# Kernel optimization log

Hardware: AMD Instinct MI355X
Metric: run time of the kernel (lower is better)

Reference implementation:

```python
import jax, jax.numpy as jnp
import numpy as np
from jax import lax

C = 128
HEADS = 8
HID = 256  # int(C * 2.0)
B, H, W = 8, 128, 128
EPS_LN = 1e-5
EPS_NORM = 1e-12


def _dwconv(x, w, pad):
    # x: [B,C,H,W], w: [C,1,kh,kw] depthwise
    return lax.conv_general_dilated(
        x, w, window_strides=(1, 1), padding=[(pad, pad), (pad, pad)],
        dimension_numbers=("NCHW", "OIHW", "NCHW"), feature_group_count=x.shape[1])


def _conv1x1(x, w):
    # w: [O, I] pointwise conv
    return jnp.einsum("oi,bihw->bohw", w, x)


def _layernorm_c(x, gamma, beta):
    # torch: reshape to [B, HW, C], LayerNorm over C, reshape back == LN over channel axis
    mu = jnp.mean(x, axis=1, keepdims=True)
    var = jnp.mean(jnp.square(x - mu), axis=1, keepdims=True)
    xn = (x - mu) * lax.rsqrt(var + EPS_LN)
    return xn * gamma[None, :, None, None] + beta[None, :, None, None]


def _l2norm(x):
    n = jnp.sqrt(jnp.sum(jnp.square(x), axis=-1, keepdims=True))
    return x / jnp.maximum(n, EPS_NORM)


def _mdta(x, qkv_w, qkv_dw, temperature, attn_proj):
    b, c, h, w = x.shape
    qkv = _dwconv(_conv1x1(x, qkv_w), qkv_dw, pad=1)  # [B,3C,H,W]
    q, k, v = jnp.split(qkv, 3, axis=1)
    hd = c // HEADS
    q = q.reshape(b, HEADS, hd, h * w)
    k = k.reshape(b, HEADS, hd, h * w)
    v = v.reshape(b, HEADS, hd, h * w)
    q, k = _l2norm(q), _l2norm(k)
    attn = jax.nn.softmax(jnp.einsum("bhdn,bhen->bhde", q, k) * temperature, axis=-1)
    out = jnp.einsum("bhde,bhen->bhdn", attn, v).reshape(b, c, h, w)
    return _conv1x1(out, attn_proj)


def _gdfn2(x, pin_w, c1_w, c3_w, c5_w, pout_w):
    x = _conv1x1(x, pin_w)  # [B,HID,H,W]
    x1 = x * c1_w[None, :, 0, 0, 0, None, None]  # depthwise 1x1 == per-channel scale
    x3 = _dwconv(x, c3_w, pad=1)
    x5 = _dwconv(x, c5_w, pad=2)
    g = jax.nn.gelu(x1, approximate=False)
    gated = jnp.concatenate([g * x3, g * x5], axis=1)  # [B,2*HID,H,W]
    return _conv1x1(gated, pout_w)


def setup_inputs() -> dict:
    key = jax.random.key(0)
    ks = jax.random.split(key, 12)
    s = 0.05
    return {
        "x": jax.random.normal(ks[0], (B, C, H, W), jnp.float32),
        "ln1_w": jnp.ones((C,), jnp.float32),
        "ln1_b": jnp.zeros((C,), jnp.float32),
        "qkv_w": jax.random.normal(ks[1], (3 * C, C), jnp.float32) * s,
        "qkv_dw": jax.random.normal(ks[2], (3 * C, 1, 3, 3), jnp.float32) * s,
        "temperature": jnp.ones((1, HEADS, 1, 1), jnp.float32),
        "attn_proj": jax.random.normal(ks[3], (C, C), jnp.float32) * s,
        "ln2_w": jnp.ones((C,), jnp.float32),
        "ln2_b": jnp.zeros((C,), jnp.float32),
        "pin_w": jax.random.normal(ks[4], (HID, C), jnp.float32) * s,
        "c1_w": jax.random.normal(ks[5], (HID, 1, 1, 1), jnp.float32) * s,
        "c3_w": jax.random.normal(ks[6], (HID, 1, 3, 3), jnp.float32) * s,
        "c5_w": jax.random.normal(ks[7], (HID, 1, 5, 5), jnp.float32) * s,
        "pout_w": jax.random.normal(ks[8], (C, 2 * HID), jnp.float32) * s,
    }


def reference(x, ln1_w, ln1_b, qkv_w, qkv_dw, temperature, attn_proj,
              ln2_w, ln2_b, pin_w, c1_w, c3_w, c5_w, pout_w):
    x = x + _mdta(_layernorm_c(x, ln1_w, ln1_b), qkv_w, qkv_dw, temperature, attn_proj)
    x = x + _gdfn2(_layernorm_c(x, ln2_w, ln2_b), pin_w, c1_w, c3_w, c5_w, pout_w)
    return x
```

## Files before the change

kernel.cpp:

```cpp
#include <hip/hip_runtime.h>
#include <type_traits>

typedef unsigned short ushort;
typedef unsigned int uint;
typedef __bf16 bf16x8 __attribute__((ext_vector_type(8)));
typedef unsigned short ushort8v __attribute__((ext_vector_type(8)));
typedef float f32x4 __attribute__((ext_vector_type(4)));

__device__ __forceinline__ float b2f(ushort u) {
    unsigned int x = ((unsigned int)u) << 16;
    float f;
    __builtin_memcpy(&f, &x, 4);
    return f;
}
__device__ __forceinline__ ushort f2bf(float f) {
    unsigned int x;
    __builtin_memcpy(&x, &f, 4);
    unsigned int r = x + 0x7fffu + ((x >> 16) & 1u);
    return (ushort)(r >> 16);
}
__device__ __forceinline__ float u2f_lo(uint u) {
    uint x = u << 16;
    float f;
    __builtin_memcpy(&f, &x, 4);
    return f;
}
__device__ __forceinline__ float u2f_hi(uint u) {
    uint x = u & 0xffff0000u;
    float f;
    __builtin_memcpy(&f, &x, 4);
    return f;
}
__device__ __forceinline__ uint packbf(float a, float b) {
    return (uint)f2bf(a) | ((uint)f2bf(b) << 16);
}

#define NPIX 16384
#define PSTRIDE 136

__device__ __forceinline__ size_t tadr(int b, int CH, int tile, int ch, int off) {
    return (((size_t)b * 256 + tile) * CH + ch) * 64 + off;
}
__device__ __forceinline__ size_t padr(int b, int tile, int p, int c) {
    return (((size_t)b * 256 + tile) * 64 + p) * 128 + c;
}

__device__ __forceinline__ void stage_plane(ushort* pl, const ushort* __restrict__ src,
                                            int b, int c, int CH, int tid) {
    uint* plu = (uint*)pl;
    for (int i = tid; i < 784; i += 256) {
        int idx;
        if (i < 136) idx = i;
        else if (i < 272) idx = 8840 + (i - 136);
        else {
            int j = i - 272;
            int r = (j >> 2) + 2;
            int cs = j & 3;
            idx = r * 68 + (cs == 0 ? 0 : 64 + cs);
        }
        plu[idx] = 0u;
    }
    for (int i = tid; i < 2048; i += 256) {
        int row = i >> 4, xg = (i & 15) << 3;
        int px0 = row * 128 + xg;
        uint4 v = *(const uint4*)&src[tadr(b, CH, px0 >> 6, c, px0 & 63)];
        uint* dst = (uint*)&pl[(row + 2) * PSTRIDE + xg + 2];
        dst[0] = v.x; dst[1] = v.y; dst[2] = v.z; dst[3] = v.w;
    }
    __syncthreads();
}

__device__ __forceinline__ void unpack12(const ushort* rowp, float* cc) {
    const uint* rp = (const uint*)rowp;
    uint4 u = *(const uint4*)rp;
    uint2 v = *(const uint2*)(rp + 4);
    cc[0] = u2f_lo(u.x); cc[1] = u2f_hi(u.x);
    cc[2] = u2f_lo(u.y); cc[3] = u2f_hi(u.y);
    cc[4] = u2f_lo(u.z); cc[5] = u2f_hi(u.z);
    cc[6] = u2f_lo(u.w); cc[7] = u2f_hi(u.w);
    cc[8] = u2f_lo(v.x); cc[9] = u2f_hi(v.x);
    cc[10] = u2f_lo(v.y); cc[11] = u2f_hi(v.y);
}

__global__ __launch_bounds__(256) void wcvt(const float* __restrict__ s0, ushort* __restrict__ d0, int n0,
                                            const float* __restrict__ s1, ushort* __restrict__ d1, int n1,
                                            const float* __restrict__ s2, ushort* __restrict__ d2, int n2) {
    int i = blockIdx.x * 256 + threadIdx.x;
    if (i < n0) d0[i] = f2bf(s0[i]);
    else if (i < n0 + n1) d1[i - n0] = f2bf(s1[i - n0]);
    else if (i < n0 + n1 + n2) d2[i - n0 - n1] = f2bf(s2[i - n0 - n1]);
}

template <int O>
__global__ __launch_bounds__(256) void ln_gemm_mfma(const float* __restrict__ xin,
                                                    const ushort* __restrict__ Wb,
                                                    const float* __restrict__ gamma,
                                                    const float* __restrict__ beta,
                                                    ushort* __restrict__ out) {
    __shared__ ushort xs[64][136];
    __shared__ float red[2][4][64];
    __shared__ float mu[64], rs[64];
    __shared__ float gl[128], bl[128];

    const int blk = blockIdx.x;
    const int b = blk >> 8;
    const int tile = blk & 255;
    const int tid = threadIdx.x;

    const float* xb = xin + (size_t)b * 128 * NPIX + tile * 64;
    float vx[4][8];
#pragma unroll
    for (int k = 0; k < 4; k++) {
        int i = tid + k * 256;
        int p = i & 63, cg = i >> 6;
        const float* src = xb + (size_t)(cg * 8) * NPIX + p;
#pragma unroll
        for (int j = 0; j < 8; j++) vx[k][j] = src[(size_t)j * NPIX];
    }
    if (tid < 128) {
        gl[tid] = gamma[tid];
        bl[tid] = beta[tid];
    }
#pragma unroll
    for (int k = 0; k < 4; k++) {
        int i = tid + k * 256;
        int p = i & 63, cg = i >> 6;
        ushort8v u;
#pragma unroll
        for (int j = 0; j < 8; j++) u[j] = f2bf(vx[k][j]);
        *(ushort8v*)&xs[p][cg * 8] = u;
    }
    __syncthreads();

    {
        const int p = tid & 63, part = tid >> 6;
        float s = 0.f, ss = 0.f;
#pragma unroll
        for (int q = 0; q < 4; q++) {
            ushort8v u = *(const ushort8v*)&xs[p][part * 32 + q * 8];
#pragma unroll
            for (int j = 0; j < 8; j++) {
                float v = b2f(u[j]);
                s += v;
                ss += v * v;
            }
        }
        red[0][part][p] = s;
        red[1][part][p] = ss;
    }
    __syncthreads();
    if (tid < 64) {
        float s = red[0][0][tid] + red[0][1][tid] + red[0][2][tid] + red[0][3][tid];
        float ss = red[1][0][tid] + red[1][1][tid] + red[1][2][tid] + red[1][3][tid];
        float m = s * (1.f / 128.f);
        float var = ss * (1.f / 128.f) - m * m;
        mu[tid] = m;
        rs[tid] = rsqrtf(var + 1e-5f);
    }
    __syncthreads();
    {
        const int p = tid & 63, part = tid >> 6;
        const float mp = mu[p], rp = rs[p];
#pragma unroll
        for (int q = 0; q < 4; q++) {
            int c0 = part * 32 + q * 8;
            ushort8v u = *(const ushort8v*)&xs[p][c0];
            ushort8v o;
#pragma unroll
            for (int j = 0; j < 8; j++) {
                float v = b2f(u[j]);
                o[j] = f2bf((v - mp) * rp * gl[c0 + j] + bl[c0 + j]);
            }
            *(ushort8v*)&xs[p][c0] = o;
        }
    }
    __syncthreads();

    const int wv = tid >> 6, lane = tid & 63;
    const int lr = lane & 15, lg = lane >> 4;

    bf16x8 bfr[4][4];
#pragma unroll
    for (int t = 0; t < 4; t++)
#pragma unroll
        for (int kc = 0; kc < 4; kc++)
            bfr[t][kc] = __builtin_bit_cast(bf16x8, *(const ushort8v*)&xs[t * 16 + lr][kc * 32 + lg * 8]);

    constexpr int MT = O / 64;
    bf16x8 afp[2][4];
#pragma unroll
    for (int kc = 0; kc < 4; kc++)
        afp[0][kc] = __builtin_bit_cast(bf16x8,
            *(const ushort8v*)&Wb[(size_t)(wv * 16 + lr) * 128 + kc * 32 + lg * 8]);

    f32x4 accPair[2][4];
    const int px8 = tid & 7, cb = tid >> 3;
    ushort* outp = out + tadr(b, O, tile, 0, 0);

#pragma unroll
    for (int mt = 0; mt < MT; mt++) {
        if (mt + 1 < MT) {
            const int o0n = ((mt + 1) * 4 + wv) * 16;
#pragma unroll
            for (int kc = 0; kc < 4; kc++)
                afp[(mt + 1) & 1][kc] = __builtin_bit_cast(bf16x8,
                    *(const ushort8v*)&Wb[(size_t)(o0n + lr) * 128 + kc * 32 + lg * 8]);
        }
        f32x4* acc = accPair[mt & 1];
#pragma unroll
        for (int t = 0; t < 4; t++) acc[t] = (f32x4){0.f, 0.f, 0.f, 0.f};
#pragma unroll
        for (int kc = 0; kc < 4; kc++)
#pragma unroll
            for (int t = 0; t < 4; t++)
                acc[t] = __builtin_amdgcn_mfma_f32_16x16x32_bf16(afp[mt & 1][kc], bfr[t][kc], acc[t], 0, 0, 0);

        if (mt & 1) {
            __syncthreads();
#pragma unroll
            for (int h = 0; h < 2; h++) {
                const int lc = h * 64 + wv * 16 + lg * 4;
#pragma unroll
                for (int t = 0; t < 4; t++) {
                    int px = t * 16 + lr;
                    uint2 pk;
                    pk.x = packbf(accPair[h][t][0], accPair[h][t][1]);
                    pk.y = packbf(accPair[h][t][2], accPair[h][t][3]);
                    *(uint2*)&xs[px][lc] = pk;
                }
            }
            __syncthreads();
            const int pairbase = (mt >> 1) * 128;
#pragma unroll
            for (int cc = 0; cc < 4; cc++) {
                int c = cb + cc * 32;
                ushort8v u;
#pragma unroll
                for (int j = 0; j < 8; j++) u[j] = xs[px8 * 8 + j][c];
                *(ushort8v*)&outp[(size_t)(pairbase + c) * 64 + px8 * 8] = u;
            }
        }
    }
}

__global__ __launch_bounds__(256) void dwconv3_lds(const ushort* __restrict__ in,
                                                   const float* __restrict__ wdw,
                                                   ushort* __restrict__ out, int CH) {
    __shared__ ushort pl[132 * PSTRIDE];
    const int c = blockIdx.x;
    const int b = blockIdx.y;
    const int tid = threadIdx.x;

    float w[9];
#pragma unroll
    for (int j = 0; j < 9; j++) w[j] = wdw[c * 9 + j];

    stage_plane(pl, in, b, c, CH, tid);

    const int x = (tid & 15) * 8;
    const int ybase = tid >> 4;
#pragma unroll 1
    for (int k = 0; k < 8; k++) {
        const int y = k * 16 + ybase;
        float a[8];
#pragma unroll
        for (int p = 0; p < 8; p++) a[p] = 0.f;
#pragma unroll
        for (int ky = 0; ky < 3; ky++) {
            float cc[12];
            unpack12(&pl[(y + ky + 1) * PSTRIDE + x], cc);
#pragma unroll
            for (int kx = 0; kx < 3; kx++) {
                float wv = w[ky * 3 + kx];
#pragma unroll
                for (int p = 0; p < 8; p++) a[p] += cc[p + kx + 1] * wv;
            }
        }
        const int px0 = (y << 7) + x;
        uint4 o;
        o.x = packbf(a[0], a[1]);
        o.y = packbf(a[2], a[3]);
        o.z = packbf(a[4], a[5]);
        o.w = packbf(a[6], a[7]);
        *(uint4*)&out[tadr(b, CH, px0 >> 6, c, px0 & 63)] = o;
    }
}

__global__ __launch_bounds__(256) void dw_gated(const ushort* __restrict__ t,
                                                const float* __restrict__ w3_,
                                                const float* __restrict__ w5_,
                                                const float* __restrict__ c1w,
                                                ushort* __restrict__ gated) {
    __shared__ ushort pl[132 * PSTRIDE];
    const int c = blockIdx.x;
    const int b = blockIdx.y;
    const int tid = threadIdx.x;

    float w3[9], w5[25];
#pragma unroll
    for (int j = 0; j < 9; j++) w3[j] = w3_[c * 9 + j];
#pragma unroll
    for (int j = 0; j < 25; j++) w5[j] = w5_[c * 25 + j];
    const float c1v = c1w[c];

    stage_plane(pl, t, b, c, 256, tid);

    const int x = (tid & 15) * 8;
    const int ybase = tid >> 4;
#pragma unroll 1
    for (int k = 0; k < 8; k++) {
        const int y = k * 16 + ybase;
        float a5[8], a3[8], tc[8];
#pragma unroll
        for (int p = 0; p < 8; p++) { a5[p] = 0.f; a3[p] = 0.f; }
#pragma unroll
        for (int ky = 0; ky < 5; ky++) {
            float cc[12];
            unpack12(&pl[(y + ky) * PSTRIDE + x], cc);
#pragma unroll
            for (int kx = 0; kx < 5; kx++) {
                float wv = w5[ky * 5 + kx];
#pragma unroll
                for (int p = 0; p < 8; p++) a5[p] += cc[p + kx] * wv;
            }
            if (ky >= 1 && ky <= 3) {
#pragma unroll
                for (int kx = 0; kx < 3; kx++) {
                    float wv = w3[(ky - 1) * 3 + kx];
#pragma unroll
                    for (int p = 0; p < 8; p++) a3[p] += cc[p + kx + 1] * wv;
                }
            }
            if (ky == 2) {
#pragma unroll
                for (int p = 0; p < 8; p++) tc[p] = cc[p + 2];
            }
        }
        const int px0 = (y << 7) + x;
        uint4 o3, o5;
        float g[8];
#pragma unroll
        for (int p = 0; p < 8; p++) {
            float x1 = tc[p] * c1v;
            g[p] = x1 * __builtin_amdgcn_rcpf(1.f + __expf(-1.702f * x1));
        }
        o3.x = packbf(g[0] * a3[0], g[1] * a3[1]);
        o3.y = packbf(g[2] * a3[2], g[3] * a3[3]);
        o3.z = packbf(g[4] * a3[4], g[5] * a3[5]);
        o3.w = packbf(g[6] * a3[6], g[7] * a3[7]);
        o5.x = packbf(g[0] * a5[0], g[1] * a5[1]);
        o5.y = packbf(g[2] * a5[2], g[3] * a5[3]);
        o5.z = packbf(g[4] * a5[4], g[5] * a5[5]);
        o5.w = packbf(g[6] * a5[6], g[7] * a5[7]);
        *(uint4*)&gated[tadr(b, 512, px0 >> 6, c, px0 & 63)] = o3;
        *(uint4*)&gated[tadr(b, 512, px0 >> 6, 256 + c, px0 & 63)] = o5;
    }
}

__global__ __launch_bounds__(512) void attn_M(const ushort* __restrict__ qkv,
                                              const float* __restrict__ temp,
                                              const float* __restrict__ attn_proj,
                                              ushort* __restrict__ M) {
    __shared__ float Sp[8][16][16];
    __shared__ float QSS[8][16], KSS[8][16];
    __shared__ float A[16][17];

    const int bh = blockIdx.x, b = bh >> 3, h = bh & 7;
    const int tid = threadIdx.x;
    const int w = tid >> 6, lane = tid & 63;
    const int lr = lane & 15, lg = lane >> 4;

    const size_t qbase = (((size_t)b * 256 + w * 32) * 384 + h * 16 + lr) * 64 + lg * 8;
    const size_t kbase = qbase + (size_t)128 * 64;

    f32x4 acc = {0.f, 0.f, 0.f, 0.f};
    f32x4 accq = {0.f, 0.f, 0.f, 0.f};
    f32x4 acck = {0.f, 0.f, 0.f, 0.f};
#pragma unroll 2
    for (int it = 0; it < 64; it++) {
        size_t off = (size_t)(it >> 1) * (384 * 64) + (it & 1) * 32;
        bf16x8 qf = __builtin_bit_cast(bf16x8, *(const ushort8v*)(qkv + qbase + off));
        bf16x8 kf = __builtin_bit_cast(bf16x8, *(const ushort8v*)(qkv + kbase + off));
        acc = __builtin_amdgcn_mfma_f32_16x16x32_bf16(qf, kf, acc, 0, 0, 0);
        accq = __builtin_amdgcn_mfma_f32_16x16x32_bf16(qf, qf, accq, 0, 0, 0);
        acck = __builtin_amdgcn_mfma_f32_16x16x32_bf16(kf, kf, acck, 0, 0, 0);
    }
#pragma unroll
    for (int r = 0; r < 4; r++) Sp[w][lg * 4 + r][lr] = acc[r];
    if (lg == (lr >> 2)) {
        QSS[w][lr] = accq[lr & 3];
        KSS[w][lr] = acck[lr & 3];
    }
    __syncthreads();

    if (tid < 256) {
        const int d = tid >> 4, e = tid & 15;
        float S = 0.f, q2 = 0.f, k2 = 0.f;
#pragma unroll
        for (int s = 0; s < 8; s++) {
            S += Sp[s][d][e];
            q2 += QSS[s][d];
            k2 += KSS[s][e];
        }
        float nq = fmaxf(sqrtf(q2), 1e-12f);
        float nk = fmaxf(sqrtf(k2), 1e-12f);
        float logit = S / (nq * nk) * temp[h];
        float m = logit;
        for (int off = 8; off; off >>= 1) m = fmaxf(m, __shfl_xor(m, off, 64));
        float ex = expf(logit - m);
        float sum = ex;
        for (int off = 8; off; off >>= 1) sum += __shfl_xor(sum, off, 64);
        A[d][e] = ex / sum;
    }
    __syncthreads();

    for (int i = tid; i < 2048; i += 512) {
        int o = i >> 4, ee = i & 15;
        float acc2 = 0.f;
#pragma unroll
        for (int dd = 0; dd < 16; dd++) acc2 += attn_proj[o * 128 + h * 16 + dd] * A[dd][ee];
        M[((size_t)b * 128 + o) * 128 + h * 16 + ee] = f2bf(acc2);
    }
}

__global__ __launch_bounds__(256) void mv_ln_mfma(const ushort* __restrict__ qkv,
                                                  const ushort* __restrict__ Mb16,
                                                  const float* __restrict__ x,
                                                  const ushort* __restrict__ pin_b,
                                                  const float* __restrict__ gamma,
                                                  const float* __restrict__ beta,
                                                  ushort* __restrict__ x2,
                                                  ushort* __restrict__ t_out) {
    __shared__ ushort ts[64][136];
    __shared__ float red[2][4][64];
    __shared__ float mu[64], rs[64];
    __shared__ float gl[128], bl[128];

    const int blk = blockIdx.x;
    const int b = blk >> 8;
    const int tile = blk & 255;
    const int tid = threadIdx.x;
    const int wv = tid >> 6, lane = tid & 63;
    const int lr = lane & 15, lg = lane >> 4;

    const ushort* Mb = Mb16 + (size_t)b * 128 * 128;
    bf16x8 mfr[2][4];
#pragma unroll
    for (int mt = 0; mt < 2; mt++)
#pragma unroll
        for (int kc = 0; kc < 4; kc++)
            mfr[mt][kc] = __builtin_bit_cast(bf16x8,
                *(const ushort8v*)&Mb[(size_t)((wv * 2 + mt) * 16 + lr) * 128 + kc * 32 + lg * 8]);

    const ushort* vb = qkv + tadr(b, 384, tile, 256, 0);
    ushort8v vv[4];
#pragma unroll
    for (int k = 0; k < 4; k++) {
        int idx = tid + k * 256;
        int c = idx & 127, pg = idx >> 7;
        vv[k] = *(const ushort8v*)&vb[c * 64 + pg * 8];
    }
    if (tid < 128) {
        gl[tid] = gamma[tid];
        bl[tid] = beta[tid];
    }
#pragma unroll
    for (int k = 0; k < 4; k++) {
        int idx = tid + k * 256;
        int c = idx & 127, pg = idx >> 7;
#pragma unroll
        for (int j = 0; j < 8; j++) ts[pg * 8 + j][c] = vv[k][j];
    }
    __syncthreads();

    bf16x8 bfr[4][4];
#pragma unroll
    for (int t = 0; t < 4; t++)
#pragma unroll
        for (int kc = 0; kc < 4; kc++)
            bfr[t][kc] = __builtin_bit_cast(bf16x8, *(const ushort8v*)&ts[t * 16 + lr][kc * 32 + lg * 8]);
    __syncthreads();

#pragma unroll
    for (int mt = 0; mt < 2; mt++) {
        const int o0 = (wv * 2 + mt) * 16;
        f32x4 acc[4] = {{0.f, 0.f, 0.f, 0.f}, {0.f, 0.f, 0.f, 0.f}, {0.f, 0.f, 0.f, 0.f}, {0.f, 0.f, 0.f, 0.f}};
#pragma unroll
        for (int kc = 0; kc < 4; kc++)
#pragma unroll
            for (int t = 0; t < 4; t++)
                acc[t] = __builtin_amdgcn_mfma_f32_16x16x32_bf16(mfr[mt][kc], bfr[t][kc], acc[t], 0, 0, 0);
#pragma unroll
        for (int t = 0; t < 4; t++) {
            int px = t * 16 + lr;
            const float* xp = &x[((size_t)b * 128 + o0 + lg * 4) * NPIX + tile * 64 + px];
            uint2 pk;
            pk.x = packbf(xp[0] + acc[t][0], xp[NPIX] + acc[t][1]);
            pk.y = packbf(xp[2 * NPIX] + acc[t][2], xp[3 * NPIX] + acc[t][3]);
            *(uint2*)&ts[px][o0 + lg * 4] = pk;
        }
    }

    bf16x8 pfp[2][4];
#pragma unroll
    for (int kc = 0; kc < 4; kc++)
        pfp[0][kc] = __builtin_bit_cast(bf16x8,
            *(const ushort8v*)&pin_b[(size_t)(wv * 16 + lr) * 128 + kc * 32 + lg * 8]);
    __syncthreads();

#pragma unroll
    for (int k = 0; k < 4; k++) {
        int idx = tid + k * 256;
        int p = idx >> 4, seg = idx & 15;
        uint4 v = *(const uint4*)&ts[p][seg * 8];
        *(uint4*)&x2[padr(b, tile, p, seg * 8)] = v;
    }
    {
        const int p = tid & 63, part = tid >> 6;
        float s = 0.f, ss = 0.f;
#pragma unroll
        for (int q = 0; q < 4; q++) {
            ushort8v u = *(const ushort8v*)&ts[p][part * 32 + q * 8];
#pragma unroll
            for (int j = 0; j < 8; j++) {
                float v = b2f(u[j]);
                s += v;
                ss += v * v;
            }
        }
        red[0][part][p] = s;
        red[1][part][p] = ss;
    }
    __syncthreads();
    if (tid < 64) {
        float s = red[0][0][tid] + red[0][1][tid] + red[0][2][tid] + red[0][3][tid];
        float ss = red[1][0][tid] + red[1][1][tid] + red[1][2][tid] + red[1][3][tid];
        float m = s * (1.f / 128.f);
        float var = ss * (1.f / 128.f) - m * m;
        mu[tid] = m;
        rs[tid] = rsqrtf(var + 1e-5f);
    }
    __syncthreads();
    {
        const int p = tid & 63, part = tid >> 6;
        const float mp = mu[p], rp = rs[p];
#pragma unroll
        for (int q = 0; q < 4; q++) {
            int c0 = part * 32 + q * 8;
            ushort8v u = *(const ushort8v*)&ts[p][c0];
            ushort8v o;
#pragma unroll
            for (int j = 0; j < 8; j++) {
                float v = b2f(u[j]);
                o[j] = f2bf((v - mp) * rp * gl[c0 + j] + bl[c0 + j]);
            }
            *(ushort8v*)&ts[p][c0] = o;
        }
    }
    __syncthreads();

    bf16x8 bfr2[4][4];
#pragma unroll
    for (int t = 0; t < 4; t++)
#pragma unroll
        for (int kc = 0; kc < 4; kc++)
            bfr2[t][kc] = __builtin_bit_cast(bf16x8, *(const ushort8v*)&ts[t * 16 + lr][kc * 32 + lg * 8]);

    f32x4 accPair[2][4];
    const int px8 = tid & 7, cb = tid >> 3;
    ushort* toutp = t_out + tadr(b, 256, tile, 0, 0);

#pragma unroll
    for (int mt = 0; mt < 4; mt++) {
        if (mt + 1 < 4) {
            const int o0n = ((mt + 1) * 4 + wv) * 16;
#pragma unroll
            for (int kc = 0; kc < 4; kc++)
                pfp[(mt + 1) & 1][kc] = __builtin_bit_cast(bf16x8,
                    *(const ushort8v*)&pin_b[(size_t)(o0n + lr) * 128 + kc * 32 + lg * 8]);
        }
        f32x4* acc = accPair[mt & 1];
#pragma unroll
        for (int t = 0; t < 4; t++) acc[t] = (f32x4){0.f, 0.f, 0.f, 0.f};
#pragma unroll
        for (int kc = 0; kc < 4; kc++)
#pragma unroll
            for (int t = 0; t < 4; t++)
                acc[t] = __builtin_amdgcn_mfma_f32_16x16x32_bf16(pfp[mt & 1][kc], bfr2[t][kc], acc[t], 0, 0, 0);

        if (mt & 1) {
            __syncthreads();
#pragma unroll
            for (int h = 0; h < 2; h++) {
                const int lc = h * 64 + wv * 16 + lg * 4;
#pragma unroll
                for (int t = 0; t < 4; t++) {
                    int px = t * 16 + lr;
                    uint2 pk;
                    pk.x = packbf(accPair[h][t][0], accPair[h][t][1]);
                    pk.y = packbf(accPair[h][t][2], accPair[h][t][3]);
                    *(uint2*)&ts[px][lc] = pk;
                }
            }
            __syncthreads();
            const int pairbase = (mt >> 1) * 128;
#pragma unroll
            for (int cc = 0; cc < 4; cc++) {
                int c = cb + cc * 32;
                ushort8v u;
#pragma unroll
                for (int j = 0; j < 8; j++) u[j] = ts[px8 * 8 + j][c];
                *(ushort8v*)&toutp[(size_t)(pairbase + c) * 64 + px8 * 8] = u;
            }
        }
    }
}

__global__ __launch_bounds__(256) void gdfn_mfma(const ushort* __restrict__ gated,
                                                 const ushort* __restrict__ x2,
                                                 const ushort* __restrict__ pout_b,
                                                 float* __restrict__ out) {
    __shared__ union {
        ushort gs[2][4160];
        float xf[32][129];
    } sm;

    const int blk = blockIdx.x;
    const int b = blk >> 8;
    const int tile = blk & 255;
    const int tid = threadIdx.x;
    const int wv = tid >> 6, lane = tid & 63;
    const int lr = lane & 15, lg = lane >> 4;

    const ushort* gb = gated + tadr(b, 512, tile, 0, 0);
    const int sdst = (tid & 3) * 1040 + (tid >> 2) * 16;

    const uint lbase = (uint)(uintptr_t)&sm.gs[0][0] + lg * 256 + lr * 2;

    f32x4 acc[2][4];
#pragma unroll
    for (int mt = 0; mt < 2; mt++)
#pragma unroll
        for (int tt = 0; tt < 4; tt++) acc[mt][tt] = (f32x4){0.f, 0.f, 0.f, 0.f};

    {
        uint4 a0 = *(const uint4*)&gb[tid * 16];
        uint4 a1 = *(const uint4*)&gb[tid * 16 + 8];
        *(uint4*)&sm.gs[0][sdst] = a0;
        *(uint4*)&sm.gs[0][sdst + 8] = a1;
    }
    __syncthreads();

#pragma unroll
    for (int kb = 0; kb < 8; kb++) {
        const int cur = kb & 1;

        uint4 nA, nB;
        if (kb < 7) {
            nA = *(const uint4*)&gb[(kb + 1) * 4096 + tid * 16];
            nB = *(const uint4*)&gb[(kb + 1) * 4096 + tid * 16 + 8];
        }

        bf16x8 bfrg[4][2];
        {
            const uint la = lbase + cur * 8320;
#pragma unroll
            for (int tt = 0; tt < 4; tt++)
#pragma unroll
                for (int kc = 0; kc < 2; kc++) {
                    uint2 r0, r1;
                    asm volatile("ds_read_b64_tr_b16 %0, %2 offset:%3\n\t"
                                 "ds_read_b64_tr_b16 %1, %2 offset:%4"
                                 : "=&v"(r0), "=&v"(r1)
                                 : "v"(la), "i"(tt * 2080 + kc * 1024), "i"(tt * 2080 + kc * 1024 + 128));
                    uint4 q;
                    q.x = r0.x; q.y = r0.y; q.z = r1.x; q.w = r1.y;
                    bfrg[tt][kc] = __builtin_bit_cast(bf16x8, q);
                }
        }
        asm volatile("s_waitcnt lgkmcnt(0)" ::: "memory");
        __builtin_amdgcn_sched_barrier(0);

#pragma unroll
        for (int mt = 0; mt < 2; mt++) {
            const int o0 = (wv * 2 + mt) * 16;
            bf16x8 afr[2];
#pragma unroll
            for (int kc = 0; kc < 2; kc++)
                afr[kc] = __builtin_bit_cast(bf16x8,
                    *(const ushort8v*)&pout_b[(size_t)(o0 + lr) * 512 + kb * 64 + kc * 32 + lg * 8]);
#pragma unroll
            for (int kc = 0; kc < 2; kc++)
#pragma unroll
                for (int tt = 0; tt < 4; tt++)
                    acc[mt][tt] = __builtin_amdgcn_mfma_f32_16x16x32_bf16(afr[kc], bfrg[tt][kc], acc[mt][tt], 0, 0, 0);
        }

        if (kb < 7) {
            *(uint4*)&sm.gs[cur ^ 1][sdst] = nA;
            *(uint4*)&sm.gs[cur ^ 1][sdst + 8] = nB;
        }
        __syncthreads();
    }

#pragma unroll
    for (int h = 0; h < 2; h++) {
#pragma unroll
        for (int mt = 0; mt < 2; mt++)
#pragma unroll
            for (int t2 = 0; t2 < 2; t2++) {
                const int tt = h * 2 + t2;
                int o0 = (wv * 2 + mt) * 16 + lg * 4;
                int px = tt * 16 + lr;
                uint2 xw = *(const uint2*)&x2[padr(b, tile, px, o0)];
                sm.xf[px - h * 32][o0 + 0] = u2f_lo(xw.x) + acc[mt][tt][0];
                sm.xf[px - h * 32][o0 + 1] = u2f_hi(xw.x) + acc[mt][tt][1];
                sm.xf[px - h * 32][o0 + 2] = u2f_lo(xw.y) + acc[mt][tt][2];
                sm.xf[px - h * 32][o0 + 3] = u2f_hi(xw.y) + acc[mt][tt][3];
            }
        __syncthreads();
        {
            const int qx = tid & 7;
            const int cbase = tid >> 3;
#pragma unroll
            for (int cc = 0; cc < 4; cc++) {
                int c = cbase + cc * 32;
                float4 v;
                v.x = sm.xf[qx * 4 + 0][c];
                v.y = sm.xf[qx * 4 + 1][c];
                v.z = sm.xf[qx * 4 + 2][c];
                v.w = sm.xf[qx * 4 + 3][c];
                *(float4*)&out[((size_t)b * 128 + c) * NPIX + tile * 64 + h * 32 + qx * 4] = v;
            }
        }
        __syncthreads();
    }
}

extern "C" void kernel_launch(void* const* d_in, const int* in_sizes, int n_in,
                              void* d_out, int out_size, void* d_ws, size_t ws_size,
                              hipStream_t stream) {
    const float* x = (const float*)d_in[0];
    const float* ln1_w = (const float*)d_in[1];
    const float* ln1_b = (const float*)d_in[2];
    const float* qkv_w = (const float*)d_in[3];
    const float* qkv_dw = (const float*)d_in[4];
    const float* temperature = (const float*)d_in[5];
    const float* attn_proj = (const float*)d_in[6];
    const float* ln2_w = (const float*)d_in[7];
    const float* ln2_b = (const float*)d_in[8];
    const float* pin_w = (const float*)d_in[9];
    const float* c1_w = (const float*)d_in[10];
    const float* c3_w = (const float*)d_in[11];
    const float* c5_w = (const float*)d_in[12];
    const float* pout_w = (const float*)d_in[13];
    float* out = (float*)d_out;

    char* ws = (char*)d_ws;
    ushort* qkv_pre = (ushort*)(ws + 0);
    ushort* qkv     = (ushort*)(ws + 100663296);
    ushort* x2      = (ushort*)(ws + 201326592);
    ushort* t       = (ushort*)(ws + 0);
    ushort* gated   = (ushort*)(ws + 67108864);
    ushort* Mb16    = (ushort*)(ws + 235151360);
    ushort* qkv_wb  = (ushort*)(ws + 235413504);
    ushort* pin_wb  = (ushort*)(ws + 235511808);
    ushort* pout_wb = (ushort*)(ws + 235577344);

    wcvt<<<576, 256, 0, stream>>>(qkv_w, qkv_wb, 49152, pin_w, pin_wb, 32768, pout_w, pout_wb, 65536);
    ln_gemm_mfma<384><<<2048, 256, 0, stream>>>(x, qkv_wb, ln1_w, ln1_b, qkv_pre);
    dwconv3_lds<<<dim3(384, 8), 256, 0, stream>>>(qkv_pre, qkv_dw, qkv, 384);
    attn_M<<<64, 512, 0, stream>>>(qkv, temperature, attn_proj, Mb16);
    mv_ln_mfma<<<2048, 256, 0, stream>>>(qkv, Mb16, x, pin_wb, ln2_w, ln2_b, x2, t);
    dw_gated<<<dim3(256, 8), 256, 0, stream>>>(t, c3_w, c5_w, c1_w, gated);
    gdfn_mfma<<<2048, 256, 0, stream>>>(gated, x2, pout_wb, out);
}
```

Measured before the change: 297.7 us.

## Fuse depthwise gated conv into GDFN output GEMM, dropping gated buffer

Merges the depthwise 3x3/5x5 gated-GELU kernel into the output pointwise MFMA GEMM. Each workgroup now stages a 5-row halo of the t tensor for its half-row tile into LDS in 64-channel chunks, computes the gated values in registers, writes them to LDS and feeds them straight into the MFMA. This removes the 128MB-scale write and re-read of the gated intermediate and one kernel launch. In exchange, halo rows are re-read from global memory by neighbouring tiles, the pipelined double-buffered global prefetch is lost, and a block-index swizzle is added for locality.

```diff
diff --git a/kernel.cpp b/kernel.cpp
--- a/kernel.cpp
+++ b/kernel.cpp
@@ -82,6 +82,23 @@
     cc[10] = u2f_lo(v.y); cc[11] = u2f_hi(v.y);
 }
 
+__device__ __forceinline__ void unpack24(const ushort* rowp, float* cv) {
+    const uint4* rp = (const uint4*)rowp;
+    uint4 u0 = rp[0], u1 = rp[1], u2 = rp[2];
+    cv[0] = u2f_lo(u0.x); cv[1] = u2f_hi(u0.x);
+    cv[2] = u2f_lo(u0.y); cv[3] = u2f_hi(u0.y);
+    cv[4] = u2f_lo(u0.z); cv[5] = u2f_hi(u0.z);
+    cv[6] = u2f_lo(u0.w); cv[7] = u2f_hi(u0.w);
+    cv[8] = u2f_lo(u1.x); cv[9] = u2f_hi(u1.x);
+    cv[10] = u2f_lo(u1.y); cv[11] = u2f_hi(u1.y);
+    cv[12] = u2f_lo(u1.z); cv[13] = u2f_hi(u1.z);
+    cv[14] = u2f_lo(u1.w); cv[15] = u2f_hi(u1.w);
+    cv[16] = u2f_lo(u2.x); cv[17] = u2f_hi(u2.x);
+    cv[18] = u2f_lo(u2.y); cv[19] = u2f_hi(u2.y);
+    cv[20] = u2f_lo(u2.z); cv[21] = u2f_hi(u2.z);
+    cv[22] = u2f_lo(u2.w); cv[23] = u2f_hi(u2.w);
+}
+
 __global__ __launch_bounds__(256) void wcvt(const float* __restrict__ s0, ushort* __restrict__ d0, int n0,
                                             const float* __restrict__ s1, ushort* __restrict__ d1, int n1,
                                             const float* __restrict__ s2, ushort* __restrict__ d2, int n2) {
@@ -283,77 +300,6 @@
         o.z = packbf(a[4], a[5]);
         o.w = packbf(a[6], a[7]);
         *(uint4*)&out[tadr(b, CH, px0 >> 6, c, px0 & 63)] = o;
-    }
-}
-
-__global__ __launch_bounds__(256) void dw_gated(const ushort* __restrict__ t,
-                                                const float* __restrict__ w3_,
-                                                const float* __restrict__ w5_,
-                                                const float* __restrict__ c1w,
-                                                ushort* __restrict__ gated) {
-    __shared__ ushort pl[132 * PSTRIDE];
-    const int c = blockIdx.x;
-    const int b = blockIdx.y;
-    const int tid = threadIdx.x;
-
-    float w3[9], w5[25];
-#pragma unroll
-    for (int j = 0; j < 9; j++) w3[j] = w3_[c * 9 + j];
-#pragma unroll
-    for (int j = 0; j < 25; j++) w5[j] = w5_[c * 25 + j];
-    const float c1v = c1w[c];
-
-    stage_plane(pl, t, b, c, 256, tid);
-
-    const int x = (tid & 15) * 8;
-    const int ybase = tid >> 4;
-#pragma unroll 1
-    for (int k = 0; k < 8; k++) {
-        const int y = k * 16 + ybase;
-        float a5[8], a3[8], tc[8];
-#pragma unroll
-        for (int p = 0; p < 8; p++) { a5[p] = 0.f; a3[p] = 0.f; }
-#pragma unroll
-        for (int ky = 0; ky < 5; ky++) {
-            float cc[12];
-            unpack12(&pl[(y + ky) * PSTRIDE + x], cc);
-#pragma unroll
-            for (int kx = 0; kx < 5; kx++) {
-                float wv = w5[ky * 5 + kx];
-#pragma unroll
-                for (int p = 0; p < 8; p++) a5[p] += cc[p + kx] * wv;
-            }
-            if (ky >= 1 && ky <= 3) {
-#pragma unroll
-                for (int kx = 0; kx < 3; kx++) {
-                    float wv = w3[(ky - 1) * 3 + kx];
-#pragma unroll
-                    for (int p = 0; p < 8; p++) a3[p] += cc[p + kx + 1] * wv;
-                }
-            }
-            if (ky == 2) {
-#pragma unroll
-                for (int p = 0; p < 8; p++) tc[p] = cc[p + 2];
-            }
-        }
-        const int px0 = (y << 7) + x;
-        uint4 o3, o5;
-        float g[8];
-#pragma unroll
-        for (int p = 0; p < 8; p++) {
-            float x1 = tc[p] * c1v;
-            g[p] = x1 * __builtin_amdgcn_rcpf(1.f + __expf(-1.702f * x1));
-        }
-        o3.x = packbf(g[0] * a3[0], g[1] * a3[1]);
-        o3.y = packbf(g[2] * a3[2], g[3] * a3[3]);
-        o3.z = packbf(g[4] * a3[4], g[5] * a3[5]);
-        o3.w = packbf(g[6] * a3[6], g[7] * a3[7]);
-        o5.x = packbf(g[0] * a5[0], g[1] * a5[1]);
-        o5.y = packbf(g[2] * a5[2], g[3] * a5[3]);
-        o5.z = packbf(g[4] * a5[4], g[5] * a5[5]);
-        o5.w = packbf(g[6] * a5[6], g[7] * a5[7]);
-        *(uint4*)&gated[tadr(b, 512, px0 >> 6, c, px0 & 63)] = o3;
-        *(uint4*)&gated[tadr(b, 512, px0 >> 6, 256 + c, px0 & 63)] = o5;
     }
 }
 
@@ -616,26 +562,29 @@
     }
 }
 
-__global__ __launch_bounds__(256) void gdfn_mfma(const ushort* __restrict__ gated,
-                                                 const ushort* __restrict__ x2,
-                                                 const ushort* __restrict__ pout_b,
-                                                 float* __restrict__ out) {
+__global__ __launch_bounds__(256) void dw_gdfn_fused(const ushort* __restrict__ t,
+                                                     const float* __restrict__ w3_,
+                                                     const float* __restrict__ w5_,
+                                                     const float* __restrict__ c1w,
+                                                     const ushort* __restrict__ x2,
+                                                     const ushort* __restrict__ pout_b,
+                                                     float* __restrict__ out) {
     __shared__ union {
-        ushort gs[2][4160];
+        ushort th[64][5][72];
         float xf[32][129];
-    } sm;
-
-    const int blk = blockIdx.x;
-    const int b = blk >> 8;
-    const int tile = blk & 255;
+    } smA;
+    __shared__ ushort tb[2][4][1040];
+
+    const int blk0 = blockIdx.x;
+    const int wg = (blk0 & 7) * 256 + (blk0 >> 3);
+    const int b = wg >> 8, tile = wg & 255;
+    const int y = tile >> 1, h = tile & 1;
     const int tid = threadIdx.x;
     const int wv = tid >> 6, lane = tid & 63;
     const int lr = lane & 15, lg = lane >> 4;
-
-    const ushort* gb = gated + tadr(b, 512, tile, 0, 0);
-    const int sdst = (tid & 3) * 1040 + (tid >> 2) * 16;
-
-    const uint lbase = (uint)(uintptr_t)&sm.gs[0][0] + lg * 256 + lr * 2;
+    const int ci = tid >> 2, g = tid & 3;
+
+    const uint lbase = (uint)(uintptr_t)&tb[0][0][0] + lg * 256 + lr * 2;
 
     f32x4 acc[2][4];
 #pragma unroll
@@ -643,27 +592,87 @@
 #pragma unroll
         for (int tt = 0; tt < 4; tt++) acc[mt][tt] = (f32x4){0.f, 0.f, 0.f, 0.f};
 
-    {
-        uint4 a0 = *(const uint4*)&gb[tid * 16];
-        uint4 a1 = *(const uint4*)&gb[tid * 16 + 8];
-        *(uint4*)&sm.gs[0][sdst] = a0;
-        *(uint4*)&sm.gs[0][sdst + 8] = a1;
-    }
-    __syncthreads();
-
-#pragma unroll
-    for (int kb = 0; kb < 8; kb++) {
-        const int cur = kb & 1;
-
-        uint4 nA, nB;
-        if (kb < 7) {
-            nA = *(const uint4*)&gb[(kb + 1) * 4096 + tid * 16];
-            nB = *(const uint4*)&gb[(kb + 1) * 4096 + tid * 16 + 8];
-        }
-
-        bf16x8 bfrg[4][2];
+#pragma unroll 1
+    for (int cc = 0; cc < 4; cc++) {
+        __syncthreads();
+        for (int i = tid; i < 320; i += 256) {
+            int sci = i & 63, r = i >> 6;
+            int yr = y + r - 2;
+            ushort* dst = &smA.th[sci][r][0];
+            uint* d4 = (uint*)dst;
+            if (yr < 0 || yr > 127) {
+                uint4 z = {0u, 0u, 0u, 0u};
+#pragma unroll
+                for (int k = 0; k < 9; k++) ((uint4*)dst)[k] = z;
+            } else {
+                int c = cc * 64 + sci;
+                const ushort* rowc = t + tadr(b, 256, yr * 2 + h, c, 0);
+                d4[0] = (h == 0) ? 0u : *(const uint*)(t + tadr(b, 256, yr * 2, c, 62));
+#pragma unroll
+                for (int k = 0; k < 8; k++) {
+                    uint4 v = *(const uint4*)&rowc[k * 8];
+                    d4[1 + k * 4] = v.x; d4[2 + k * 4] = v.y;
+                    d4[3 + k * 4] = v.z; d4[4 + k * 4] = v.w;
+                }
+                d4[33] = (h == 1) ? 0u : *(const uint*)(t + tadr(b, 256, yr * 2 + 1, c, 0));
+                d4[34] = 0u; d4[35] = 0u;
+            }
+        }
+        __syncthreads();
         {
-            const uint la = lbase + cur * 8320;
+            const int c = cc * 64 + ci;
+            float w5r[25], w3r[9];
+#pragma unroll
+            for (int j = 0; j < 25; j++) w5r[j] = w5_[c * 25 + j];
+#pragma unroll
+            for (int j = 0; j < 9; j++) w3r[j] = w3_[c * 9 + j];
+            const float c1v = c1w[c];
+            float a5[16], a3[16], tcv[16];
+#pragma unroll
+            for (int j = 0; j < 16; j++) { a5[j] = 0.f; a3[j] = 0.f; }
+#pragma unroll
+            for (int r = 0; r < 5; r++) {
+                float cv[24];
+                unpack24(&smA.th[ci][r][g * 16], cv);
+#pragma unroll
+                for (int kx = 0; kx < 5; kx++) {
+                    float w = w5r[r * 5 + kx];
+#pragma unroll
+                    for (int j = 0; j < 16; j++) a5[j] += cv[j + kx] * w;
+                }
+                if (r >= 1 && r <= 3) {
+#pragma unroll
+                    for (int kx = 0; kx < 3; kx++) {
+                        float w = w3r[(r - 1) * 3 + kx];
+#pragma unroll
+                        for (int j = 0; j < 16; j++) a3[j] += cv[j + 1 + kx] * w;
+                    }
+                }
+                if (r == 2) {
+#pragma unroll
+                    for (int j = 0; j < 16; j++) tcv[j] = cv[j + 2];
+                }
+            }
+            ushort8v o3a, o3b, o5a, o5b;
+#pragma unroll
+            for (int j = 0; j < 16; j++) {
+                float x1 = tcv[j] * c1v;
+                float gg = x1 * __builtin_amdgcn_rcpf(1.f + __expf(-1.702f * x1));
+                ushort v3 = f2bf(gg * a3[j]);
+                ushort v5 = f2bf(gg * a5[j]);
+                if (j < 8) { o3a[j] = v3; o5a[j] = v5; }
+                else { o3b[j - 8] = v3; o5b[j - 8] = v5; }
+            }
+            *(ushort8v*)&tb[0][g][ci * 16] = o3a;
+            *(ushort8v*)&tb[0][g][ci * 16 + 8] = o3b;
+            *(ushort8v*)&tb[1][g][ci * 16] = o5a;
+            *(ushort8v*)&tb[1][g][ci * 16 + 8] = o5b;
+        }
+        __syncthreads();
+#pragma unroll
+        for (int hh = 0; hh < 2; hh++) {
+            bf16x8 bfrg[4][2];
+            const uint la = lbase + hh * 8320;
 #pragma unroll
             for (int tt = 0; tt < 4; tt++)
 #pragma unroll
@@ -677,60 +686,55 @@
                     q.x = r0.x; q.y = r0.y; q.z = r1.x; q.w = r1.y;
                     bfrg[tt][kc] = __builtin_bit_cast(bf16x8, q);
                 }
-        }
-        asm volatile("s_waitcnt lgkmcnt(0)" ::: "memory");
-        __builtin_amdgcn_sched_barrier(0);
-
-#pragma unroll
-        for (int mt = 0; mt < 2; mt++) {
-            const int o0 = (wv * 2 + mt) * 16;
-            bf16x8 afr[2];
-#pragma unroll
-            for (int kc = 0; kc < 2; kc++)
-                afr[kc] = __builtin_bit_cast(bf16x8,
-                    *(const ushort8v*)&pout_b[(size_t)(o0 + lr) * 512 + kb * 64 + kc * 32 + lg * 8]);
-#pragma unroll
-            for (int kc = 0; kc < 2; kc++)
-#pragma unroll
-                for (int tt = 0; tt < 4; tt++)
-                    acc[mt][tt] = __builtin_amdgcn_mfma_f32_16x16x32_bf16(afr[kc], bfrg[tt][kc], acc[mt][tt], 0, 0, 0);
-        }
-
-        if (kb < 7) {
-            *(uint4*)&sm.gs[cur ^ 1][sdst] = nA;
-            *(uint4*)&sm.gs[cur ^ 1][sdst + 8] = nB;
-        }
-        __syncthreads();
-    }
-
-#pragma unroll
-    for (int h = 0; h < 2; h++) {
+            asm volatile("s_waitcnt lgkmcnt(0)" ::: "memory");
+            __builtin_amdgcn_sched_barrier(0);
+
+#pragma unroll
+            for (int mt = 0; mt < 2; mt++) {
+                const int o0 = (wv * 2 + mt) * 16;
+                bf16x8 afr[2];
+#pragma unroll
+                for (int kc = 0; kc < 2; kc++)
+                    afr[kc] = __builtin_bit_cast(bf16x8,
+                        *(const ushort8v*)&pout_b[(size_t)(o0 + lr) * 512 + hh * 256 + cc * 64 + kc * 32 + lg * 8]);
+#pragma unroll
+                for (int kc = 0; kc < 2; kc++)
+#pragma unroll
+                    for (int tt = 0; tt < 4; tt++)
+                        acc[mt][tt] = __builtin_amdgcn_mfma_f32_16x16x32_bf16(afr[kc], bfrg[tt][kc], acc[mt][tt], 0, 0, 0);
+            }
+        }
+    }
+    __syncthreads();
+
+#pragma unroll
+    for (int hf = 0; hf < 2; hf++) {
 #pragma unroll
         for (int mt = 0; mt < 2; mt++)
 #pragma unroll
             for (int t2 = 0; t2 < 2; t2++) {
-                const int tt = h * 2 + t2;
+                const int tt = hf * 2 + t2;
                 int o0 = (wv * 2 + mt) * 16 + lg * 4;
                 int px = tt * 16 + lr;
                 uint2 xw = *(const uint2*)&x2[padr(b, tile, px, o0)];
-                sm.xf[px - h * 32][o0 + 0] = u2f_lo(xw.x) + acc[mt][tt][0];
-                sm.xf[px - h * 32][o0 + 1] = u2f_hi(xw.x) + acc[mt][tt][1];
-                sm.xf[px - h * 32][o0 + 2] = u2f_lo(xw.y) + acc[mt][tt][2];
-                sm.xf[px - h * 32][o0 + 3] = u2f_hi(xw.y) + acc[mt][tt][3];
+                smA.xf[px - hf * 32][o0 + 0] = u2f_lo(xw.x) + acc[mt][tt][0];
+                smA.xf[px - hf * 32][o0 + 1] = u2f_hi(xw.x) + acc[mt][tt][1];
+                smA.xf[px - hf * 32][o0 + 2] = u2f_lo(xw.y) + acc[mt][tt][2];
+                smA.xf[px - hf * 32][o0 + 3] = u2f_hi(xw.y) + acc[mt][tt][3];
             }
         __syncthreads();
         {
             const int qx = tid & 7;
             const int cbase = tid >> 3;
 #pragma unroll
-            for (int cc = 0; cc < 4; cc++) {
-                int c = cbase + cc * 32;
+            for (int cc2 = 0; cc2 < 4; cc2++) {
+                int c = cbase + cc2 * 32;
                 float4 v;
-                v.x = sm.xf[qx * 4 + 0][c];
-                v.y = sm.xf[qx * 4 + 1][c];
-                v.z = sm.xf[qx * 4 + 2][c];
-                v.w = sm.xf[qx * 4 + 3][c];
-                *(float4*)&out[((size_t)b * 128 + c) * NPIX + tile * 64 + h * 32 + qx * 4] = v;
+                v.x = smA.xf[qx * 4 + 0][c];
+                v.y = smA.xf[qx * 4 + 1][c];
+                v.z = smA.xf[qx * 4 + 2][c];
+                v.w = smA.xf[qx * 4 + 3][c];
+                *(float4*)&out[((size_t)b * 128 + c) * NPIX + tile * 64 + hf * 32 + qx * 4] = v;
             }
         }
         __syncthreads();
@@ -761,7 +765,6 @@
     ushort* qkv     = (ushort*)(ws + 100663296);
     ushort* x2      = (ushort*)(ws + 201326592);
     ushort* t       = (ushort*)(ws + 0);
-    ushort* gated   = (ushort*)(ws + 67108864);
     ushort* Mb16    = (ushort*)(ws + 235151360);
     ushort* qkv_wb  = (ushort*)(ws + 235413504);
     ushort* pin_wb  = (ushort*)(ws + 235511808);
@@ -772,6 +775,5 @@
     dwconv3_lds<<<dim3(384, 8), 256, 0, stream>>>(qkv_pre, qkv_dw, qkv, 384);
     attn_M<<<64, 512, 0, stream>>>(qkv, temperature, attn_proj, Mb16);
     mv_ln_mfma<<<2048, 256, 0, stream>>>(qkv, Mb16, x, pin_wb, ln2_w, ln2_b, x2, t);
-    dw_gated<<<dim3(256, 8), 256, 0, stream>>>(t, c3_w, c5_w, c1_w, gated);
-    gdfn_mfma<<<2048, 256, 0, stream>>>(gated, x2, pout_wb, out);
-}
+    dw_gdfn_fused<<<2048, 256, 0, stream>>>(t, c3_w, c5_w, c1_w, x2, pout_wb, out);
+}
```

After: 373.3 us, median of 2. 1.25x slower.
